# Performance work log

Hardware: AMD Instinct MI355X
Metric: run time of the kernel (lower is better)

The kernel has to match this reference:

```python
import jax, jax.numpy as jnp
import numpy as np

M, K, N = 64, 4096, 14336


def setup_inputs() -> dict:
    key = jax.random.key(0)
    k1, k2, k3, k4, k5 = jax.random.split(key, 5)
    x = jax.random.normal(k1, (M, K), dtype=jnp.float32)
    # int8-valued weights stored as int32 (values in [-128, 128))
    weight = jax.random.randint(k2, (K, N), -128, 128, dtype=jnp.int32)
    # per-channel dequant params (one per output channel N)
    antiquant_scale = jax.random.uniform(k3, (N,), dtype=jnp.float32, minval=0.001, maxval=0.02)
    antiquant_offset = jax.random.normal(k4, (N,), dtype=jnp.float32)
    bias = jax.random.normal(k5, (N,), dtype=jnp.float32)
    return {"x": x, "weight": weight, "antiquant_scale": antiquant_scale,
            "antiquant_offset": antiquant_offset, "bias": bias}


def reference(x, weight, antiquant_scale, antiquant_offset, bias):
    # npu_weight_quant_batchmatmul, per-channel antiquant, no output quant:
    # out = x @ ((weight + antiquant_offset) * antiquant_scale) + bias
    w_deq = (weight.astype(x.dtype) + antiquant_offset[None, :]) * antiquant_scale[None, :]  # [K, N]
    out = jnp.einsum('mk,kn->mn', x, w_deq) + bias[None, :]  # [M, N]
    return out
```

## Files before the change

kernel.cpp:

```cpp
#include <hip/hip_runtime.h>
#include <hip/hip_bf16.h>

#define M_DIM 64
#define K_DIM 4096
#define N_DIM 14336
#define NBLKS 224
#define KW 512
#define WCHUNKS 16

typedef __attribute__((ext_vector_type(8))) short bf16x8;
typedef __attribute__((ext_vector_type(4))) float f32x4;
typedef unsigned short u16;

__global__ __launch_bounds__(128) void prep_split(
    const float* __restrict__ x, u16* __restrict__ xh, u16* __restrict__ xl) {
  int tg = blockIdx.x * 128 + threadIdx.x;
  int kb = tg & 511;
  int m = tg >> 9;
  const float* xp = x + m * K_DIM + kb * 8;
  u16 hs[8], ls[8];
#pragma unroll
  for (int j = 0; j < 8; ++j) {
    float v = xp[j];
    unsigned hv = __float_as_uint(v) & 0xFFFF0000u;
    float r = v - __uint_as_float(hv);
    hs[j] = (u16)(hv >> 16);
    ls[j] = (u16)(__float_as_uint(r) >> 16);
  }
  int o = kb * (M_DIM * 8) + m * 8;
  *(uint4*)(xh + o) = *(uint4*)hs;
  *(uint4*)(xl + o) = *(uint4*)ls;
}

__global__ __launch_bounds__(512, 2) void wqmm(
    const int* __restrict__ W, const u16* __restrict__ xh,
    const u16* __restrict__ xl, const float* __restrict__ scale,
    const float* __restrict__ offset, const float* __restrict__ bias,
    float* __restrict__ out) {
  __shared__ __align__(16) float red[4][64][66];

  const int t = threadIdx.x;
  const int lane = t & 63;
  const int wv = t >> 6;
  const int quad = lane >> 4;
  const int lnk = lane & 15;
  const int nbase = blockIdx.x * 64;
  const int k0 = wv * KW;

  int laneoff[4];
#pragma unroll
  for (int f = 0; f < 4; ++f)
    laneoff[f] = quad * 8 * N_DIM + nbase + lnk + f * 16;

  const u16* xhp = xh + (size_t)(wv * 64 + quad) * 512 + lnk * 8;
  const u16* xlp = xl + (size_t)(wv * 64 + quad) * 512 + lnk * 8;

  const bf16x8 bones = {(short)0x3F80, (short)0x3F80, (short)0x3F80,
                        (short)0x3F80, (short)0x3F80, (short)0x3F80,
                        (short)0x3F80, (short)0x3F80};

  f32x4 acc[4][4] = {};
  f32x4 acc1[4] = {};
  int raw[2][4][8];
  bf16x8 abh[2][4], abl[2][4];

#define LOADW(CC, BUF)                                            \
  do {                                                            \
    _Pragma("unroll") for (int j = 0; j < 8; ++j) {               \
      const int* bj = W + (size_t)(k0 + (CC) * 32 + j) * N_DIM;   \
      _Pragma("unroll") for (int f = 0; f < 4; ++f)               \
          raw[BUF][f][j] = bj[laneoff[f]];                        \
    }                                                             \
  } while (0)

#define LOADA(CC, BUF)                                            \
  do {                                                            \
    const u16* ahc = xhp + (CC) * 2048;                           \
    const u16* alc = xlp + (CC) * 2048;                           \
    _Pragma("unroll") for (int mt = 0; mt < 4; ++mt) {            \
      abh[BUF][mt] = *(const bf16x8*)(ahc + mt * 128);            \
      abl[BUF][mt] = *(const bf16x8*)(alc + mt * 128);            \
    }                                                             \
  } while (0)

#define COMPUTE(CC, BUF)                                                     \
  do {                                                                       \
    bf16x8 bfr[4];                                                           \
    _Pragma("unroll") for (int f = 0; f < 4; ++f) {                          \
      union {                                                                \
        int i4[4];                                                           \
        bf16x8 v;                                                            \
      } u;                                                                   \
      _Pragma("unroll") for (int wd = 0; wd < 4; ++wd) {                     \
        unsigned lo = __float_as_uint((float)raw[BUF][f][2 * wd]);           \
        unsigned hi = __float_as_uint((float)raw[BUF][f][2 * wd + 1]);       \
               \
        u.i4[wd] = (int)__builtin_amdgcn_perm(hi, lo, 0x07060302u);          \
      }                                                                      \
      bfr[f] = u.v;                                                          \
    }                                                                        \
    _Pragma("unroll") for (int mt = 0; mt < 4; ++mt) {                       \
      _Pragma("unroll") for (int f = 0; f < 4; ++f) {                        \
        acc[mt][f] = __builtin_amdgcn_mfma_f32_16x16x32_bf16(                \
            abh[BUF][mt], bfr[f], acc[mt][f], 0, 0, 0);                      \
        acc[mt][f] = __builtin_amdgcn_mfma_f32_16x16x32_bf16(                \
            abl[BUF][mt], bfr[f], acc[mt][f], 0, 0, 0);                      \
      }                                                                      \
      acc1[mt] = __builtin_amdgcn_mfma_f32_16x16x32_bf16(                    \
          abh[BUF][mt], bones, acc1[mt], 0, 0, 0);                           \
      acc1[mt] = __builtin_amdgcn_mfma_f32_16x16x32_bf16(                    \
          abl[BUF][mt], bones, acc1[mt], 0, 0, 0);                           \
    }                                                                        \
  } while (0)

  LOADW(0, 0);
  LOADA(0, 0);
  for (int c = 0; c < WCHUNKS; c += 2) {
    LOADW(c + 1, 1);
    LOADA(c + 1, 1);
    COMPUTE(c, 0);
    if (c + 2 < WCHUNKS) {
      LOADW(c + 2, 0);
      LOADA(c + 2, 0);
    }
    COMPUTE(c + 1, 1);
  }
#undef LOADW
#undef LOADA
#undef COMPUTE

  if (wv < 4) {
#pragma unroll
    for (int f = 0; f < 4; ++f)
#pragma unroll
      for (int mt = 0; mt < 4; ++mt)
#pragma unroll
        for (int r = 0; r < 4; ++r)
          red[wv][mt * 16 + quad * 4 + r][f * 16 + lnk] = acc[mt][f][r];
    if (lnk == 0) {
#pragma unroll
      for (int mt = 0; mt < 4; ++mt)
#pragma unroll
        for (int r = 0; r < 4; ++r)
          red[wv][mt * 16 + quad * 4 + r][64] = acc1[mt][r];
    }
  }
  __syncthreads();
  if (wv >= 4) {
#pragma unroll
    for (int f = 0; f < 4; ++f)
#pragma unroll
      for (int mt = 0; mt < 4; ++mt)
#pragma unroll
        for (int r = 0; r < 4; ++r)
          red[wv - 4][mt * 16 + quad * 4 + r][f * 16 + lnk] += acc[mt][f][r];
    if (lnk == 0) {
#pragma unroll
      for (int mt = 0; mt < 4; ++mt)
#pragma unroll
        for (int r = 0; r < 4; ++r)
          red[wv - 4][mt * 16 + quad * 4 + r][64] += acc1[mt][r];
    }
  }
  __syncthreads();

#pragma unroll
  for (int i = 0; i < 8; ++i) {
    int idx = t + i * 512;
    int m = idx >> 6;
    int nc = idx & 63;
    float s = red[0][m][nc] + red[1][m][nc] + red[2][m][nc] + red[3][m][nc];
    float rs = red[0][m][64] + red[1][m][64] + red[2][m][64] + red[3][m][64];
    int n = nbase + nc;
    float sc = scale[n];
    out[(size_t)m * N_DIM + n] = s * sc + sc * offset[n] * rs + bias[n];
  }
}

extern "C" void kernel_launch(void* const* d_in, const int* in_sizes, int n_in,
                              void* d_out, int out_size, void* d_ws,
                              size_t ws_size, hipStream_t stream) {
  const float* x = (const float*)d_in[0];
  const int* W = (const int*)d_in[1];
  const float* scale = (const float*)d_in[2];
  const float* offset = (const float*)d_in[3];
  const float* bias = (const float*)d_in[4];
  float* out = (float*)d_out;

  char* wsb = (char*)d_ws;
  u16* xh = (u16*)wsb;
  u16* xl = xh + (size_t)M_DIM * K_DIM;

  prep_split<<<256, 128, 0, stream>>>(x, xh, xl);
  wqmm<<<NBLKS, 512, 0, stream>>>(W, xh, xl, scale, offset, bias, out);
}
```

Before: 334.0 us.

## Vectorize int32 weight loads, interleave K chunks across waves, deepen prefetch

Each lane now loads four adjacent weight columns with a single 16-byte vector load instead of four scalar loads strided by 16 columns. The output column mapping is permuted to match, and the epilogue index is remapped accordingly. K chunks are interleaved across the eight waves rather than each wave owning a contiguous K slice, so concurrent waves read neighbouring rows. The loop is restructured into separate pack and MMA stages with loads issued two chunks ahead, which aims to hide memory latency better. The cost is more registers held for in-flight buffers.

```diff
diff --git a/kernel.cpp b/kernel.cpp
--- a/kernel.cpp
+++ b/kernel.cpp
@@ -5,11 +5,11 @@
 #define K_DIM 4096
 #define N_DIM 14336
 #define NBLKS 224
-#define KW 512
 #define WCHUNKS 16
 
 typedef __attribute__((ext_vector_type(8))) short bf16x8;
 typedef __attribute__((ext_vector_type(4))) float f32x4;
+typedef __attribute__((ext_vector_type(4))) int i32x4;
 typedef unsigned short u16;
 
 __global__ __launch_bounds__(128) void prep_split(
@@ -45,15 +45,10 @@
   const int quad = lane >> 4;
   const int lnk = lane & 15;
   const int nbase = blockIdx.x * 64;
-  const int k0 = wv * KW;
 
-  int laneoff[4];
-#pragma unroll
-  for (int f = 0; f < 4; ++f)
-    laneoff[f] = quad * 8 * N_DIM + nbase + lnk + f * 16;
-
-  const u16* xhp = xh + (size_t)(wv * 64 + quad) * 512 + lnk * 8;
-  const u16* xlp = xl + (size_t)(wv * 64 + quad) * 512 + lnk * 8;
+  const int wcol = nbase + 4 * lnk;
+  const u16* xhp = xh + (size_t)(wv * 4 + quad) * 512 + lnk * 8;
+  const u16* xlp = xl + (size_t)(wv * 4 + quad) * 512 + lnk * 8;
 
   const bf16x8 bones = {(short)0x3F80, (short)0x3F80, (short)0x3F80,
                         (short)0x3F80, (short)0x3F80, (short)0x3F80,
@@ -61,44 +56,47 @@
 
   f32x4 acc[4][4] = {};
   f32x4 acc1[4] = {};
-  int raw[2][4][8];
+  __align__(16) int rw[2][8][4];
   bf16x8 abh[2][4], abl[2][4];
+  bf16x8 bfr[4];
 
-#define LOADW(CC, BUF)                                            \
-  do {                                                            \
-    _Pragma("unroll") for (int j = 0; j < 8; ++j) {               \
-      const int* bj = W + (size_t)(k0 + (CC) * 32 + j) * N_DIM;   \
-      _Pragma("unroll") for (int f = 0; f < 4; ++f)               \
-          raw[BUF][f][j] = bj[laneoff[f]];                        \
-    }                                                             \
+#define LOADW(CC, BUF)                                                     \
+  do {                                                                     \
+    const int* bp =                                                        \
+        W + (size_t)((wv + 8 * (CC)) * 32 + quad * 8) * N_DIM + wcol;      \
+    _Pragma("unroll") for (int j = 0; j < 8; ++j)                          \
+        *(i32x4*)rw[BUF][j] = *(const i32x4*)(bp + (size_t)j * N_DIM);     \
   } while (0)
 
 #define LOADA(CC, BUF)                                            \
   do {                                                            \
-    const u16* ahc = xhp + (CC) * 2048;                           \
-    const u16* alc = xlp + (CC) * 2048;                           \
+    const u16* ahc = xhp + (size_t)(CC) * 16384;                  \
+    const u16* alc = xlp + (size_t)(CC) * 16384;                  \
     _Pragma("unroll") for (int mt = 0; mt < 4; ++mt) {            \
       abh[BUF][mt] = *(const bf16x8*)(ahc + mt * 128);            \
       abl[BUF][mt] = *(const bf16x8*)(alc + mt * 128);            \
     }                                                             \
   } while (0)
 
-#define COMPUTE(CC, BUF)                                                     \
+#define PACK(BUF)                                                            \
   do {                                                                       \
-    bf16x8 bfr[4];                                                           \
     _Pragma("unroll") for (int f = 0; f < 4; ++f) {                          \
       union {                                                                \
         int i4[4];                                                           \
         bf16x8 v;                                                            \
       } u;                                                                   \
       _Pragma("unroll") for (int wd = 0; wd < 4; ++wd) {                     \
-        unsigned lo = __float_as_uint((float)raw[BUF][f][2 * wd]);           \
-        unsigned hi = __float_as_uint((float)raw[BUF][f][2 * wd + 1]);       \
+        unsigned lo = __float_as_uint((float)rw[BUF][2 * wd][f]);            \
+        unsigned hi = __float_as_uint((float)rw[BUF][2 * wd + 1][f]);        \
                \
         u.i4[wd] = (int)__builtin_amdgcn_perm(hi, lo, 0x07060302u);          \
       }                                                                      \
       bfr[f] = u.v;                                                          \
     }                                                                        \
+  } while (0)
+
+#define MMA(BUF)                                                             \
+  do {                                                                       \
     _Pragma("unroll") for (int mt = 0; mt < 4; ++mt) {                       \
       _Pragma("unroll") for (int f = 0; f < 4; ++f) {                        \
         acc[mt][f] = __builtin_amdgcn_mfma_f32_16x16x32_bf16(                \
@@ -115,19 +113,22 @@
 
   LOADW(0, 0);
   LOADA(0, 0);
+  LOADW(1, 1);
+  LOADA(1, 1);
   for (int c = 0; c < WCHUNKS; c += 2) {
-    LOADW(c + 1, 1);
-    LOADA(c + 1, 1);
-    COMPUTE(c, 0);
-    if (c + 2 < WCHUNKS) {
-      LOADW(c + 2, 0);
-      LOADA(c + 2, 0);
-    }
-    COMPUTE(c + 1, 1);
+    PACK(0);
+    if (c + 2 < WCHUNKS) LOADW(c + 2, 0);
+    MMA(0);
+    if (c + 2 < WCHUNKS) LOADA(c + 2, 0);
+    PACK(1);
+    if (c + 3 < WCHUNKS) LOADW(c + 3, 1);
+    MMA(1);
+    if (c + 3 < WCHUNKS) LOADA(c + 3, 1);
   }
 #undef LOADW
 #undef LOADA
-#undef COMPUTE
+#undef PACK
+#undef MMA
 
   if (wv < 4) {
 #pragma unroll
@@ -171,7 +172,7 @@
     int nc = idx & 63;
     float s = red[0][m][nc] + red[1][m][nc] + red[2][m][nc] + red[3][m][nc];
     float rs = red[0][m][64] + red[1][m][64] + red[2][m][64] + red[3][m][64];
-    int n = nbase + nc;
+    int n = nbase + 4 * (nc & 15) + (nc >> 4);
     float sc = scale[n];
     out[(size_t)m * N_DIM + n] = s * sc + sc * offset[n] * rs + bias[n];
   }
```

After: 337.2 us. No clear change (+1.0%).
